# Kernel optimization log

Measured on AMD Instinct MI355X. Metric: run time of the kernel, lower is better.

## Reference

```python
import jax, jax.numpy as jnp
import numpy as np

N_NODES = 100000


def _gcn_layer(h, W, b, src, dst, norm, n):
    # h: [N, Fin] -> transform then normalized scatter-add aggregation
    h = h @ W                                   # [N, Fout]
    msg = h[src] * norm[:, None]                # [E', Fout] gather + scale
    out = jax.ops.segment_sum(msg, dst, num_segments=n)  # scatter-add
    return out + b


def setup_inputs() -> dict:
    key = jax.random.key(0)
    k1, k2, k3, k4 = jax.random.split(key, 4)
    N, F_IN, HID, C, E = N_NODES, 512, 128, 40, 1600000
    x = jax.random.normal(k1, (N, F_IN), dtype=jnp.float32)
    edge_index = jax.random.randint(k2, (2, E), 0, N, dtype=jnp.int64)
    W1 = jax.random.normal(k3, (F_IN, HID), dtype=jnp.float32) * (1.0 / np.sqrt(F_IN))
    b1 = jnp.zeros((HID,), dtype=jnp.float32)
    W2 = jax.random.normal(k4, (HID, C), dtype=jnp.float32) * (1.0 / np.sqrt(HID))
    b2 = jnp.zeros((C,), dtype=jnp.float32)
    return {"x": x, "edge_index": edge_index, "W1": W1, "b1": b1, "W2": W2, "b2": b2}


def reference(x, edge_index, W1, b1, W2, b2):
    n = x.shape[0]
    # add self-loops (GCNConv default)
    loop = jnp.arange(n, dtype=edge_index.dtype)
    src = jnp.concatenate([edge_index[0], loop])
    dst = jnp.concatenate([edge_index[1], loop])
    # symmetric normalization: deg counted on destination (in-degree, incl. self-loop)
    deg = jax.ops.segment_sum(jnp.ones_like(dst, dtype=x.dtype), dst, num_segments=n)
    dis = jnp.where(deg > 0, jax.lax.rsqrt(deg), 0.0)  # deg^{-1/2}
    norm = dis[src] * dis[dst]                          # per-edge weight

    h = jax.nn.relu(_gcn_layer(x, W1, b1, src, dst, norm, n))
    # dropout: identity in eval mode (training=False)
    h = _gcn_layer(h, W2, b2, src, dst, norm, n)
    return jax.nn.log_softmax(h, axis=1)
```

## Files before the change

kernel.cpp:

```cpp
#include <hip/hip_runtime.h>
#include <hip/hip_bf16.h>


#define F_IN 512
#define HID  128
#define NC   40
#define NCP  48

typedef __attribute__((ext_vector_type(8))) short bf16x8;
typedef __attribute__((ext_vector_type(4))) float f32x4v;

__device__ __forceinline__ ushort f2bf(float f) {
    unsigned r;
    asm("v_cvt_pk_bf16_f32 %0, %1, %1" : "=v"(r) : "v"(f));
    return (ushort)r;
}
__device__ __forceinline__ unsigned cvtpk(float a, float b) {
    unsigned r;
    asm("v_cvt_pk_bf16_f32 %0, %1, %2" : "=v"(r) : "v"(a), "v"(b));
    return r;
}
__device__ __forceinline__ float bf2f(ushort u) {
    return __uint_as_float((unsigned)u << 16);
}
__device__ __forceinline__ bf16x8 cvt8(float4 lo, float4 hi) {
    union { unsigned u[4]; bf16x8 v; } t;
    t.u[0] = cvtpk(lo.x, lo.y); t.u[1] = cvtpk(lo.z, lo.w);
    t.u[2] = cvtpk(hi.x, hi.y); t.u[3] = cvtpk(hi.z, hi.w);
    return t.v;
}

__global__ void prep_k(const int* __restrict__ dst, int E, int EB,
                       unsigned* __restrict__ cnt, int* __restrict__ rank,
                       const float* __restrict__ W1, const float* __restrict__ W2,
                       ushort* __restrict__ W1p, ushort* __restrict__ W2p) {
    int b = blockIdx.x;
    if (b < EB) {
        int t = b * 256 + threadIdx.x;
        if (t < E) rank[t] = (int)atomicAdd(&cnt[dst[t]], 1u);
        return;
    }
    int t = (b - EB) * 256 + threadIdx.x;
    if (t < 65536) {
        int j = t & 7, n = (t >> 3) & 127, kb = (t >> 10) & 3, s = t >> 12;
        int k = s * 32 + kb * 8 + j;
        W1p[t] = f2bf(W1[(size_t)k * HID + n]);
    } else {
        int q = t - 65536;
        if (q < 6144) {
            int j = q & 7;
            int i2 = q >> 3;
            int n = i2 % 48;
            int i3 = i2 / 48;
            int kb = i3 & 3, ks = i3 >> 2;
            int k = ks * 32 + kb * 8 + j;
            float v = (n < NC) ? W2[(size_t)k * NC + n] : 0.f;
            W2p[q] = f2bf(v);
        }
    }
}

__global__ __launch_bounds__(1024) void scan_block(const unsigned* __restrict__ cnt,
                                                   unsigned* __restrict__ offs,
                                                   unsigned* __restrict__ bsums,
                                                   float* __restrict__ dis, int N) {
    int tid = threadIdx.x;
    int i = blockIdx.x * 1024 + tid;
    unsigned v = (i < N) ? cnt[i] : 0u;
    if (i < N) dis[i] = rsqrtf((float)v + 1.0f);
    int lane = tid & 63, w = tid >> 6;
    unsigned s = v;
    #pragma unroll
    for (int d = 1; d < 64; d <<= 1) {
        unsigned t = __shfl_up(s, d, 64);
        if (lane >= d) s += t;
    }
    __shared__ unsigned wt[16];
    if (lane == 63) wt[w] = s;
    __syncthreads();
    unsigned add = 0;
    #pragma unroll
    for (int j = 0; j < 16; j++) add += (j < w) ? wt[j] : 0u;
    unsigned incl = s + add;
    if (i < N) offs[i] = incl - v;
    if (tid == 1023) bsums[blockIdx.x] = incl;
}

__global__ __launch_bounds__(1024) void scan_add2(unsigned* __restrict__ offs,
                                                  const unsigned* __restrict__ bsums,
                                                  int N, unsigned total) {
    int i = blockIdx.x * 1024 + threadIdx.x;
    int lane = threadIdx.x & 63;
    unsigned s = 0;
    for (int j = lane; j < (int)blockIdx.x; j += 64) s += bsums[j];
    #pragma unroll
    for (int d = 1; d < 64; d <<= 1) s += __shfl_xor(s, d, 64);
    if (i < N) offs[i] += s;
    if (i == 0) offs[N] = total;
}

__global__ __launch_bounds__(256, 3) void fill_gemm1(
        const int* __restrict__ src, const int* __restrict__ dst,
        const unsigned* __restrict__ offs, const int* __restrict__ rank,
        int* __restrict__ col, int E, int GB,
        const float* __restrict__ A, const ushort* __restrict__ Bp,
        const float* __restrict__ dis, ushort* __restrict__ C, int N) {
    const int bid = blockIdx.x;
    const int g   = bid / 5;
    const int r5  = bid - g * 5;
    if (!(r5 == 0 && g < GB)) {
        int gb_before = g + (r5 > 0 ? 1 : 0);
        if (gb_before > GB) gb_before = GB;
        int t = (bid - gb_before) * 256 + threadIdx.x;
        if (t < E) {
            int d = dst[t];
            col[offs[d] + (unsigned)rank[t]] = src[t];
        }
        return;
    }
    const int tid  = threadIdx.x;
    const int wave = tid >> 6;
    const int lane = tid & 63;
    const int quad = lane >> 4;
    const int mr   = lane & 15;
    const int base = (g * 4 + wave) * 16;
    if (base >= N) return;
    const int r0 = base + mr;
    const float* ap0 = A + (size_t)(r0 < N ? r0 : 0) * F_IN + quad * 8;
    const ushort* bp = Bp + quad * 1024 + mr * 8;

    f32x4v acc0[8];
    #pragma unroll
    for (int t = 0; t < 8; t++) acc0[t] = (f32x4v){0.f, 0.f, 0.f, 0.f};

    #pragma unroll 1
    for (int h = 0; h < 2; h++) {
        float4 av[8][2];
        #pragma unroll
        for (int q = 0; q < 8; q++) {
            av[q][0] = *(const float4*)(ap0 + (h * 8 + q) * 32);
            av[q][1] = *(const float4*)(ap0 + (h * 8 + q) * 32 + 4);
        }
        bf16x8 af[8];
        #pragma unroll
        for (int q = 0; q < 8; q++) af[q] = cvt8(av[q][0], av[q][1]);
        #pragma unroll
        for (int s2 = 0; s2 < 8; s2++) {
            const ushort* bs = bp + (h * 8 + s2) * 4096;
            #pragma unroll
            for (int t = 0; t < 8; t++) {
                bf16x8 bb = *(const bf16x8*)(bs + t * 128);
                acc0[t] = __builtin_amdgcn_mfma_f32_16x16x32_bf16(af[s2], bb, acc0[t], 0, 0, 0);
            }
        }
    }

    #pragma unroll
    for (int rr = 0; rr < 4; rr++) {
        int ra = base + quad * 4 + rr;
        if (ra < N) {
            float ds = dis[ra];
            #pragma unroll
            for (int t = 0; t < 8; t++)
                C[(size_t)ra * HID + t * 16 + mr] = f2bf(acc0[t][rr] * ds);
        }
    }
}

__global__ __launch_bounds__(256) void agg1_k(const ushort* __restrict__ h,
                                              const int* __restrict__ col,
                                              const unsigned* __restrict__ offs,
                                              const float* __restrict__ dis,
                                              const float* __restrict__ b1,
                                              ushort* __restrict__ out, int N) {
    int node = blockIdx.x * 4 + (threadIdx.x >> 6);
    if (node >= N) return;
    int lane = threadIdx.x & 63;
    int ni = lane >> 4;
    int fl = lane & 15;
    const ushort* hb = h + (size_t)fl * 8;
    float a[8] = {0.f, 0.f, 0.f, 0.f, 0.f, 0.f, 0.f, 0.f};
    if (ni == 0) {
        uint4 v = *(const uint4*)(hb + (size_t)node * HID);
        const ushort* u = (const ushort*)&v;
        #pragma unroll
        for (int j = 0; j < 8; j++) a[j] = bf2f(u[j]);
    }
    unsigned p0 = offs[node], p1 = offs[node + 1];
    int s0, s1, s2, s3;
    float w0, w1, w2, w3;
    #define GETC1(pos, sv, wv) { unsigned q_ = (pos); bool v_ = q_ < p1; \
        sv = v_ ? col[q_] : 0; wv = v_ ? 1.f : 0.f; }
    GETC1(p0 + ni,      s0, w0);
    GETC1(p0 + ni + 4,  s1, w1);
    GETC1(p0 + ni + 8,  s2, w2);
    GETC1(p0 + ni + 12, s3, w3);
    for (unsigned p = p0; p < p1; p += 16) {
        int n0, n1, n2, n3;
        float x0, x1, x2, x3;
        GETC1(p + 16 + ni, n0, x0);
        GETC1(p + 20 + ni, n1, x1);
        GETC1(p + 24 + ni, n2, x2);
        GETC1(p + 28 + ni, n3, x3);
        uint4 v0 = *(const uint4*)(hb + (size_t)s0 * HID);
        uint4 v1 = *(const uint4*)(hb + (size_t)s1 * HID);
        uint4 v2 = *(const uint4*)(hb + (size_t)s2 * HID);
        uint4 v3 = *(const uint4*)(hb + (size_t)s3 * HID);
        const ushort* u0 = (const ushort*)&v0;
        const ushort* u1 = (const ushort*)&v1;
        const ushort* u2 = (const ushort*)&v2;
        const ushort* u3 = (const ushort*)&v3;
        #pragma unroll
        for (int j = 0; j < 8; j++)
            a[j] += (w0 * bf2f(u0[j]) + w1 * bf2f(u1[j]))
                  + (w2 * bf2f(u2[j]) + w3 * bf2f(u3[j]));
        s0 = n0; w0 = x0; s1 = n1; w1 = x1;
        s2 = n2; w2 = x2; s3 = n3; w3 = x3;
    }
    #pragma unroll
    for (int j = 0; j < 8; j++) {
        a[j] += __shfl_xor(a[j], 16);
        a[j] += __shfl_xor(a[j], 32);
    }
    if (ni == 0) {
        float dd = dis[node];
        float4 bb0 = *(const float4*)(b1 + fl * 8);
        float4 bb1 = *(const float4*)(b1 + fl * 8 + 4);
        const float bb[8] = {bb0.x, bb0.y, bb0.z, bb0.w, bb1.x, bb1.y, bb1.z, bb1.w};
        __align__(16) ushort o[8];
        #pragma unroll
        for (int j = 0; j < 8; j++) o[j] = f2bf(fmaxf(a[j] * dd + bb[j], 0.f));
        *(uint4*)(out + (size_t)node * HID + (size_t)fl * 8) = *(const uint4*)o;
    }
}

__global__ __launch_bounds__(256) void gemm2_mfma(const ushort* __restrict__ A,
                                                  const ushort* __restrict__ W2p,
                                                  const float* __restrict__ dis,
                                                  ushort* __restrict__ h2, int N) {
    const int tid  = threadIdx.x;
    const int wave = tid >> 6;
    const int lane = tid & 63;
    const int quad = lane >> 4;
    const int mr   = lane & 15;
    const int base = (blockIdx.x * 4 + wave) * 32;
    if (base >= N) return;
    const int r0 = base + mr;
    const int r1 = base + 16 + mr;
    const bool ok0 = r0 < N, ok1 = r1 < N;
    const ushort* ap0 = A + (size_t)(ok0 ? r0 : 0) * HID + quad * 8;
    const ushort* ap1 = A + (size_t)(ok1 ? r1 : 0) * HID + quad * 8;
    const ushort* bp = W2p + quad * 384 + mr * 8;

    f32x4v acc0[3], acc1[3];
    #pragma unroll
    for (int t = 0; t < 3; t++) {
        acc0[t] = (f32x4v){0.f, 0.f, 0.f, 0.f};
        acc1[t] = (f32x4v){0.f, 0.f, 0.f, 0.f};
    }
    #pragma unroll
    for (int ks = 0; ks < 4; ks++) {
        bf16x8 a0 = *(const bf16x8*)(ap0 + ks * 32);
        bf16x8 a1 = *(const bf16x8*)(ap1 + ks * 32);
        #pragma unroll
        for (int t = 0; t < 3; t++) {
            bf16x8 b = *(const bf16x8*)(bp + ks * 1536 + t * 128);
            acc0[t] = __builtin_amdgcn_mfma_f32_16x16x32_bf16(a0, b, acc0[t], 0, 0, 0);
            acc1[t] = __builtin_amdgcn_mfma_f32_16x16x32_bf16(a1, b, acc1[t], 0, 0, 0);
        }
    }
    #pragma unroll
    for (int rr = 0; rr < 4; rr++) {
        int ra = base + quad * 4 + rr;
        if (ra < N) {
            float ds = dis[ra];
            #pragma unroll
            for (int t = 0; t < 3; t++) {
                int c = t * 16 + mr;
                if (c < NC) h2[(size_t)ra * NCP + c] = f2bf(acc0[t][rr] * ds);
            }
        }
        int rb = base + 16 + quad * 4 + rr;
        if (rb < N) {
            float ds = dis[rb];
            #pragma unroll
            for (int t = 0; t < 3; t++) {
                int c = t * 16 + mr;
                if (c < NC) h2[(size_t)rb * NCP + c] = f2bf(acc1[t][rr] * ds);
            }
        }
    }
}

__global__ __launch_bounds__(256) void agg2_ls(const ushort* __restrict__ h2,
                                               const int* __restrict__ col,
                                               const unsigned* __restrict__ offs,
                                               const float* __restrict__ dis,
                                               const float* __restrict__ b2,
                                               float* __restrict__ out, int N) {
    int node = blockIdx.x * 4 + (threadIdx.x >> 6);
    if (node >= N) return;
    int lane = threadIdx.x & 63;
    int ni = lane >> 3;
    int fl = lane & 7;
    const bool act = fl < 5;
    const ushort* hb = h2 + (size_t)fl * 8;
    float a[8] = {0.f, 0.f, 0.f, 0.f, 0.f, 0.f, 0.f, 0.f};
    if (ni == 0 && act) {
        uint4 v = *(const uint4*)(hb + (size_t)node * NCP);
        const ushort* u = (const ushort*)&v;
        #pragma unroll
        for (int j = 0; j < 8; j++) a[j] = bf2f(u[j]);
    }
    unsigned p0 = offs[node], p1 = offs[node + 1];
    int s0, s1, s2, s3;
    float w0, w1, w2, w3;
    GETC1(p0 + ni,      s0, w0);
    GETC1(p0 + ni + 8,  s1, w1);
    GETC1(p0 + ni + 16, s2, w2);
    GETC1(p0 + ni + 24, s3, w3);
    for (unsigned p = p0; p < p1; p += 32) {
        int n0, n1, n2, n3;
        float x0, x1, x2, x3;
        GETC1(p + 32 + ni, n0, x0);
        GETC1(p + 40 + ni, n1, x1);
        GETC1(p + 48 + ni, n2, x2);
        GETC1(p + 56 + ni, n3, x3);
        if (act) {
            uint4 v0 = *(const uint4*)(hb + (size_t)s0 * NCP);
            uint4 v1 = *(const uint4*)(hb + (size_t)s1 * NCP);
            uint4 v2 = *(const uint4*)(hb + (size_t)s2 * NCP);
            uint4 v3 = *(const uint4*)(hb + (size_t)s3 * NCP);
            const ushort* u0 = (const ushort*)&v0;
            const ushort* u1 = (const ushort*)&v1;
            const ushort* u2 = (const ushort*)&v2;
            const ushort* u3 = (const ushort*)&v3;
            #pragma unroll
            for (int j = 0; j < 8; j++)
                a[j] += (w0 * bf2f(u0[j]) + w1 * bf2f(u1[j]))
                      + (w2 * bf2f(u2[j]) + w3 * bf2f(u3[j]));
        }
        s0 = n0; w0 = x0; s1 = n1; w1 = x1;
        s2 = n2; w2 = x2; s3 = n3; w3 = x3;
    }
    #pragma unroll
    for (int j = 0; j < 8; j++) {
        a[j] += __shfl_xor(a[j], 8);
        a[j] += __shfl_xor(a[j], 16);
        a[j] += __shfl_xor(a[j], 32);
    }
    float dd = dis[node];
    float l[8];
    float m = -1e30f;
    if (act) {
        #pragma unroll
        for (int j = 0; j < 8; j++) {
            l[j] = a[j] * dd + b2[fl * 8 + j];
            m = fmaxf(m, l[j]);
        }
    }
    #pragma unroll
    for (int d = 1; d < 8; d <<= 1) m = fmaxf(m, __shfl_xor(m, d, 8));
    float s = 0.f;
    if (act) {
        #pragma unroll
        for (int j = 0; j < 8; j++) s += __expf(l[j] - m);
    }
    #pragma unroll
    for (int d = 1; d < 8; d <<= 1) s += __shfl_xor(s, d, 8);
    float lse = m + __logf(s);
    if (ni == 0 && act) {
        float* op = out + (size_t)node * NC + fl * 8;
        *(float4*)op       = make_float4(l[0]-lse, l[1]-lse, l[2]-lse, l[3]-lse);
        *(float4*)(op + 4) = make_float4(l[4]-lse, l[5]-lse, l[6]-lse, l[7]-lse);
    }
}

extern "C" void kernel_launch(void* const* d_in, const int* in_sizes, int n_in,
                              void* d_out, int out_size, void* d_ws, size_t ws_size,
                              hipStream_t stream) {
    const float* x  = (const float*)d_in[0];
    const int*   ei = (const int*)d_in[1];
    const float* W1 = (const float*)d_in[2];
    const float* b1 = (const float*)d_in[3];
    const float* W2 = (const float*)d_in[4];
    const float* b2 = (const float*)d_in[5];
    float* out = (float*)d_out;

    const int N = in_sizes[0] / F_IN;
    const int E = in_sizes[1] / 2;
    const int* src = ei;
    const int* dst = ei + E;

    char* ws = (char*)d_ws;
    size_t o = 0;
    unsigned* cnt  = (unsigned*)(ws + o); o += (size_t)N * 4;
    float*    dis  = (float*)   (ws + o); o += (size_t)N * 4;
    unsigned* offs = (unsigned*)(ws + o); o += (size_t)(N + 4) * 4;
    unsigned* bsums= (unsigned*)(ws + o); o += 4096;
    int*      rank = (int*)     (ws + o); o += (size_t)E * 4;
    int*      col  = (int*)     (ws + o); o += (size_t)E * 4;
    o = (o + 15) & ~(size_t)15;
    ushort*   W1p  = (ushort*)  (ws + o); o += (size_t)F_IN * HID * 2;
    o = (o + 15) & ~(size_t)15;
    ushort*   W2p  = (ushort*)  (ws + o); o += 6144 * 2;
    o = (o + 15) & ~(size_t)15;
    ushort*   h1   = (ushort*)  (ws + o); o += (size_t)N * HID * 2;
    o = (o + 15) & ~(size_t)15;
    ushort*   ag1  = (ushort*)  (ws + o); o += (size_t)N * HID * 2;
    o = (o + 15) & ~(size_t)15;
    ushort*   h2   = (ushort*)  (ws + o); o += (size_t)N * NCP * 2;

    const int nb = (N + 1023) / 1024;
    const int EB = (E + 255) / 256;
    const int PB = (65536 + 6144 + 255) / 256;
    const int GB = (N + 63) / 64;

    hipMemsetAsync(cnt, 0, (size_t)N * 4, stream);
    prep_k<<<EB + PB, 256, 0, stream>>>(dst, E, EB, cnt, rank, W1, W2, W1p, W2p);
    scan_block<<<nb, 1024, 0, stream>>>(cnt, offs, bsums, dis, N);
    scan_add2<<<nb, 1024, 0, stream>>>(offs, bsums, N, (unsigned)E);

    fill_gemm1<<<GB + EB, 256, 0, stream>>>(src, dst, offs, rank, col, E, GB,
                                            x, W1p, dis, h1, N);

    agg1_k<<<(N + 3) / 4, 256, 0, stream>>>(h1, col, offs, dis, b1, ag1, N);

    gemm2_mfma<<<(N + 127) / 128, 256, 0, stream>>>(ag1, W2p, dis, h2, N);
    agg2_ls<<<(N + 3) / 4, 256, 0, stream>>>(h2, col, offs, dis, b2, out, N);
}
```

Measured before the change: 587.4 us.

## Stage W1 in LDS with 1024-thread blocks and rebalance fill/GEMM1 block split

The fused CSR-fill plus GEMM1 kernel now uses 1024-thread blocks that cooperatively stage the packed W1 into 64 KB of shared memory in two halves. They prefetch A rows with a rolling 4-deep register buffer, which removes the redundant per-wave global reads of B. The fill work moves to every third block using a grid-stride loop instead of one block per 256 edges. GEMM2 also stages W2 into LDS. The tradeoff is extra barriers, heavy LDS use that limits occupancy, and tail handling that now relies on clamped row indices.

```diff
diff --git a/kernel.cpp b/kernel.cpp
--- a/kernel.cpp
+++ b/kernel.cpp
@@ -99,59 +99,85 @@
     if (i == 0) offs[N] = total;
 }
 
-__global__ __launch_bounds__(256, 3) void fill_gemm1(
+__global__ __launch_bounds__(1024, 4) void fillg1(
         const int* __restrict__ src, const int* __restrict__ dst,
         const unsigned* __restrict__ offs, const int* __restrict__ rank,
-        int* __restrict__ col, int E, int GB,
+        int* __restrict__ col, int E, int F,
         const float* __restrict__ A, const ushort* __restrict__ Bp,
         const float* __restrict__ dis, ushort* __restrict__ C, int N) {
+    __shared__ ushort Bs[32768];
     const int bid = blockIdx.x;
-    const int g   = bid / 5;
-    const int r5  = bid - g * 5;
-    if (!(r5 == 0 && g < GB)) {
-        int gb_before = g + (r5 > 0 ? 1 : 0);
-        if (gb_before > GB) gb_before = GB;
-        int t = (bid - gb_before) * 256 + threadIdx.x;
-        if (t < E) {
-            int d = dst[t];
-            col[offs[d] + (unsigned)rank[t]] = src[t];
+    const int tid = threadIdx.x;
+    if (bid % 3 == 2) {
+        const int stride = F * 1024;
+        for (int e = (bid / 3) * 1024 + tid; e < E; e += stride) {
+            int d = dst[e];
+            col[offs[d] + (unsigned)rank[e]] = src[e];
         }
         return;
     }
-    const int tid  = threadIdx.x;
+    const int g    = bid - bid / 3;
     const int wave = tid >> 6;
     const int lane = tid & 63;
     const int quad = lane >> 4;
     const int mr   = lane & 15;
-    const int base = (g * 4 + wave) * 16;
-    if (base >= N) return;
+    const int base = g * 256 + wave * 16;
     const int r0 = base + mr;
     const float* ap0 = A + (size_t)(r0 < N ? r0 : 0) * F_IN + quad * 8;
-    const ushort* bp = Bp + quad * 1024 + mr * 8;
+    const ushort* lbp = Bs + quad * 1024 + mr * 8;
+
+    {
+        const uint4* bsrc = (const uint4*)Bp;
+        uint4* bdst = (uint4*)Bs;
+        #pragma unroll
+        for (int r = 0; r < 4; r++) bdst[tid + r * 1024] = bsrc[tid + r * 1024];
+    }
 
     f32x4v acc0[8];
     #pragma unroll
     for (int t = 0; t < 8; t++) acc0[t] = (f32x4v){0.f, 0.f, 0.f, 0.f};
 
-    #pragma unroll 1
-    for (int h = 0; h < 2; h++) {
-        float4 av[8][2];
-        #pragma unroll
-        for (int q = 0; q < 8; q++) {
-            av[q][0] = *(const float4*)(ap0 + (h * 8 + q) * 32);
-            av[q][1] = *(const float4*)(ap0 + (h * 8 + q) * 32 + 4);
-        }
-        bf16x8 af[8];
-        #pragma unroll
-        for (int q = 0; q < 8; q++) af[q] = cvt8(av[q][0], av[q][1]);
-        #pragma unroll
-        for (int s2 = 0; s2 < 8; s2++) {
-            const ushort* bs = bp + (h * 8 + s2) * 4096;
-            #pragma unroll
-            for (int t = 0; t < 8; t++) {
-                bf16x8 bb = *(const bf16x8*)(bs + t * 128);
-                acc0[t] = __builtin_amdgcn_mfma_f32_16x16x32_bf16(af[s2], bb, acc0[t], 0, 0, 0);
-            }
+    float4 av[4][2];
+    #pragma unroll
+    for (int b = 0; b < 4; b++) {
+        av[b][0] = *(const float4*)(ap0 + b * 32);
+        av[b][1] = *(const float4*)(ap0 + b * 32 + 4);
+    }
+    __syncthreads();
+
+    #pragma unroll
+    for (int s = 0; s < 8; s++) {
+        bf16x8 fa = cvt8(av[s & 3][0], av[s & 3][1]);
+        av[s & 3][0] = *(const float4*)(ap0 + (s + 4) * 32);
+        av[s & 3][1] = *(const float4*)(ap0 + (s + 4) * 32 + 4);
+        const ushort* bs = lbp + s * 4096;
+        #pragma unroll
+        for (int t = 0; t < 8; t++) {
+            bf16x8 bb = *(const bf16x8*)(bs + t * 128);
+            acc0[t] = __builtin_amdgcn_mfma_f32_16x16x32_bf16(fa, bb, acc0[t], 0, 0, 0);
+        }
+    }
+    __syncthreads();
+    {
+        const uint4* bsrc = (const uint4*)Bp;
+        uint4* bdst = (uint4*)Bs;
+        #pragma unroll
+        for (int r = 0; r < 4; r++) bdst[tid + r * 1024] = bsrc[4096 + tid + r * 1024];
+    }
+    __syncthreads();
+
+    #pragma unroll
+    for (int s = 8; s < 16; s++) {
+        bf16x8 fa = cvt8(av[s & 3][0], av[s & 3][1]);
+        if (s < 12) {
+            av[s & 3][0] = *(const float4*)(ap0 + (s + 4) * 32);
+            av[s & 3][1] = *(const float4*)(ap0 + (s + 4) * 32 + 4);
+        }
+        const ushort* bs = lbp + (s - 8) * 4096;
+        #pragma unroll
+        for (int t = 0; t < 8; t++) {
+            bf16x8 bb = *(const bf16x8*)(bs + t * 128);
+            acc0[t] = __builtin_amdgcn_mfma_f32_16x16x32_bf16(fa, bb, acc0[t], 0, 0, 0);
         }
     }
 
@@ -238,7 +264,15 @@
                                                   const ushort* __restrict__ W2p,
                                                   const float* __restrict__ dis,
                                                   ushort* __restrict__ h2, int N) {
+    __shared__ ushort Ws[6144];
     const int tid  = threadIdx.x;
+    {
+        const uint4* s = (const uint4*)W2p;
+        uint4* d = (uint4*)Ws;
+        #pragma unroll
+        for (int r = 0; r < 3; r++) d[tid + r * 256] = s[tid + r * 256];
+    }
+    __syncthreads();
     const int wave = tid >> 6;
     const int lane = tid & 63;
     const int quad = lane >> 4;
@@ -250,7 +284,7 @@
     const bool ok0 = r0 < N, ok1 = r1 < N;
     const ushort* ap0 = A + (size_t)(ok0 ? r0 : 0) * HID + quad * 8;
     const ushort* ap1 = A + (size_t)(ok1 ? r1 : 0) * HID + quad * 8;
-    const ushort* bp = W2p + quad * 384 + mr * 8;
+    const ushort* bp = Ws + quad * 384 + mr * 8;
 
     f32x4v acc0[3], acc1[3];
     #pragma unroll
@@ -414,15 +448,20 @@
     const int nb = (N + 1023) / 1024;
     const int EB = (E + 255) / 256;
     const int PB = (65536 + 6144 + 255) / 256;
-    const int GB = (N + 63) / 64;
+    const int GB = (N + 255) / 256;
+
+    int T = GB + GB / 2;
+    while (T - T / 3 < GB) ++T;
+    while (T - T / 3 > GB) --T;
+    const int F = T / 3;
 
     hipMemsetAsync(cnt, 0, (size_t)N * 4, stream);
     prep_k<<<EB + PB, 256, 0, stream>>>(dst, E, EB, cnt, rank, W1, W2, W1p, W2p);
     scan_block<<<nb, 1024, 0, stream>>>(cnt, offs, bsums, dis, N);
     scan_add2<<<nb, 1024, 0, stream>>>(offs, bsums, N, (unsigned)E);
 
-    fill_gemm1<<<GB + EB, 256, 0, stream>>>(src, dst, offs, rank, col, E, GB,
-                                            x, W1p, dis, h1, N);
+    fillg1<<<T, 1024, 0, stream>>>(src, dst, offs, rank, col, E, F,
+                                   x, W1p, dis, h1, N);
 
     agg1_k<<<(N + 3) / 4, 256, 0, stream>>>(h1, col, offs, dis, b1, ag1, N);
 
```

New measurement: 545.7 us. -7.1%, faster.
